# Kernel tuning notes

Measured on AMD Instinct MI355X. Metric: run time of the kernel, lower is better.

## Reference

```python
import jax, jax.numpy as jnp
import numpy as np

NUM_HEADS = 8
HEAD_DIM = 64
D_MODEL = NUM_HEADS * HEAD_DIM  # 512
B, T = 4, 2048


def setup_inputs() -> dict:
    key = jax.random.key(0)
    k1, k2 = jax.random.split(key)
    x = jax.random.normal(k1, (B, T, D_MODEL), dtype=jnp.float32)
    mask = jnp.ones((B, 1, T, T), dtype=jnp.float32)
    W = jax.random.normal(k2, (D_MODEL, 3 * D_MODEL), dtype=jnp.float32) * (D_MODEL ** -0.5)
    b = jnp.zeros((3 * D_MODEL,), dtype=jnp.float32)
    return {"x": x, "mask": mask, "W": W, "b": b}


def reference(x, mask, W, b):
    batch = x.shape[0]
    # fused QKV projection: [B, T, 3D]
    qkv = jnp.einsum("btd,de->bte", x, W) + b
    # NOTE: faithful to torch reshape [B, T, H, Hd, 3] -> the size-3 axis is innermost
    qkv = qkv.reshape(batch, -1, NUM_HEADS, HEAD_DIM, 3)
    qkv = jnp.transpose(qkv, (4, 0, 2, 1, 3))  # [3, B, H, T, Hd]
    q, k, v = qkv[0], qkv[1], qkv[2]
    logits = jnp.einsum("bhqd,bhkd->bhqk", q, k) / (HEAD_DIM ** 0.5)
    logits = logits + (1.0 - mask) * -10000.0
    w = jax.nn.softmax(logits, axis=-1)
    out = jnp.einsum("bhqk,bhkd->bhqd", w, v)  # [B, H, T, Hd]
    out = jnp.transpose(out, (0, 2, 1, 3)).reshape(batch, -1, NUM_HEADS * HEAD_DIM)
    return out
```

## Files before the change

### kernel.cpp

```cpp
#include <hip/hip_runtime.h>
#include <hip/hip_bf16.h>
#include <stdint.h>

#define B_   4
#define T_   2048
#define H_   8
#define HD_  64
#define DM_  512
#define N3_  1536

typedef short bf_el;
typedef __attribute__((ext_vector_type(8))) bf_el bfrag;
typedef __attribute__((ext_vector_type(4))) float ffrag;

#define SCALE_L2E  0.18033688011112043f
#define MASK_L2E   14426.950408889634f

static __device__ __forceinline__ unsigned short f2bf(float f) {
    union { float f; unsigned int i; } v; v.f = f;
    unsigned int r = v.i + 0x7fff + ((v.i >> 16) & 1);
    return (unsigned short)(r >> 16);
}
static __device__ __forceinline__ unsigned short f2bf_fast(float f) {
    union { float f; unsigned int i; } v; v.f = f;
    return (unsigned short)((v.i + 0x8000u) >> 16);
}

__global__ __launch_bounds__(256) void k_prep(const float* __restrict__ W,
                                              const float* __restrict__ X,
                                              const float* __restrict__ mask,
                                              unsigned short* __restrict__ Wt,
                                              unsigned short* __restrict__ Xb,
                                              int* __restrict__ flags4) {
    __shared__ __align__(16) unsigned short Ls[64 * 72];
    const int bid = blockIdx.x;
    const int tid = threadIdx.x;

    if (bid < 512) {
        const int R0 = bid * 16;
        const int mb = R0 >> 11;
        const int q0 = R0 & 2047;
        const int e  = mb * 32 + (q0 >> 6);
        const int part = (R0 >> 4) & 3;
        const int wave = tid >> 6, lane = tid & 63;
        unsigned int acc = 0u;
        const float* base = mask + (size_t)R0 * T_ + tid * 8;
#pragma unroll
        for (int rr = 0; rr < 16; ++rr) {
            const uint4 u0 = *(const uint4*)(base + (size_t)rr * T_);
            const uint4 u1 = *(const uint4*)(base + (size_t)rr * T_ + 4);
            acc |= (u0.x ^ 0x3F800000u) | (u0.y ^ 0x3F800000u) |
                   (u0.z ^ 0x3F800000u) | (u0.w ^ 0x3F800000u) |
                   (u1.x ^ 0x3F800000u) | (u1.y ^ 0x3F800000u) |
                   (u1.z ^ 0x3F800000u) | (u1.w ^ 0x3F800000u);
        }
        unsigned long long bal = __ballot(acc != 0u);
        if (lane < 8) {
            const int kt = wave * 8 + lane;
            flags4[(e * 32 + kt) * 4 + part] = ((bal >> (8 * lane)) & 0xFFULL) ? 1 : 0;
        }
        return;
    }
    if (bid < 768) {
        const int b2 = bid - 512;
        const float* src = X + (size_t)b2 * 16384;
        unsigned short* dst = Xb + (size_t)b2 * 16384;
#pragma unroll
        for (int j = 0; j < 8; ++j) {
            int idx = j * 512 + tid * 2;
            float4 f0 = *(const float4*)(src + idx * 4);
            float4 f1 = *(const float4*)(src + idx * 4 + 4);
            __align__(16) unsigned short t8[8];
            t8[0] = f2bf_fast(f0.x); t8[1] = f2bf_fast(f0.y);
            t8[2] = f2bf_fast(f0.z); t8[3] = f2bf_fast(f0.w);
            t8[4] = f2bf_fast(f1.x); t8[5] = f2bf_fast(f1.y);
            t8[6] = f2bf_fast(f1.z); t8[7] = f2bf_fast(f1.w);
            *(uint4*)(dst + idx * 4) = *(const uint4*)t8;
        }
        return;
    }
    {
        const int t  = bid - 768;
        const int n0 = (t % 24) * 64;
        const int k0 = (t / 24) * 64;
#pragma unroll
        for (int i = 0; i < 4; ++i) {
            int chunk = tid + i * 256;
            int k = chunk >> 4;
            int c = chunk & 15;
            float4 f = *(const float4*)(W + (size_t)(k0 + k) * N3_ + n0 + c * 4);
            unsigned short* p = Ls + k * 72 + c * 4;
            p[0] = f2bf(f.x); p[1] = f2bf(f.y); p[2] = f2bf(f.z); p[3] = f2bf(f.w);
        }
        __syncthreads();
        const int n = tid >> 2;
        const int g = tid & 3;
        __align__(16) unsigned short tmp[16];
#pragma unroll
        for (int i = 0; i < 16; ++i) tmp[i] = Ls[(g * 16 + i) * 72 + n];
        uint4* dst = (uint4*)(Wt + (size_t)(n0 + n) * DM_ + k0 + g * 16);
        dst[0] = *(const uint4*)(tmp);
        dst[1] = *(const uint4*)(tmp + 8);
    }
}

__global__ __launch_bounds__(256, 4) void k_gemm_qkv(const unsigned short* __restrict__ Xb,
                                                     const unsigned short* __restrict__ Wt,
                                                     const float* __restrict__ bias,
                                                     unsigned short* __restrict__ Qb,
                                                     unsigned short* __restrict__ Kb,
                                                     unsigned short* __restrict__ Vtb) {
    __shared__ __align__(16) unsigned short SH[12800];
    unsigned short* As = SH;
    unsigned short* Bs = SH + 2560;
    unsigned short* Cs = SH;

    const int tid  = threadIdx.x;
    const int wave = tid >> 6;
    const int lane = tid & 63;
    const int quad = lane >> 4;
    const int l16  = lane & 15;
    const int wm = wave >> 1, wn = wave & 1;
    const int h  = blockIdx.x >> 7;
    const int m0 = (blockIdx.x & 127) * 64;
    const int n0 = h * 192;

    float bvv[6];
#pragma unroll
    for (int ni = 0; ni < 6; ++ni) bvv[ni] = bias[n0 + wn * 96 + ni * 16 + l16];

    ffrag acc[2][6];
#pragma unroll
    for (int i = 0; i < 2; ++i)
#pragma unroll
        for (int j = 0; j < 6; ++j) acc[i][j] = (ffrag){0.f, 0.f, 0.f, 0.f};

    const int ar = tid >> 2, ac = tid & 3;
    const int br0 = tid >> 2, br1 = (tid + 256) >> 2, br2 = (tid + 512) >> 2;
    const int bc  = tid & 3;
    uint4 pa, pb0, pb1, pb2;

    pa  = *(const uint4*)(Xb + (size_t)(m0 + ar) * DM_ + ac * 8);
    pb0 = *(const uint4*)(Wt + (size_t)(n0 + br0) * DM_ + bc * 8);
    pb1 = *(const uint4*)(Wt + (size_t)(n0 + br1) * DM_ + bc * 8);
    pb2 = *(const uint4*)(Wt + (size_t)(n0 + br2) * DM_ + bc * 8);

    for (int kt = 0; kt < 16; ++kt) {
        __syncthreads();
        *(uint4*)(As + ar * 40 + ac * 8)  = pa;
        *(uint4*)(Bs + br0 * 40 + bc * 8) = pb0;
        *(uint4*)(Bs + br1 * 40 + bc * 8) = pb1;
        *(uint4*)(Bs + br2 * 40 + bc * 8) = pb2;
        __syncthreads();
        if (kt < 15) {
            const int ko = (kt + 1) * 32;
            pa  = *(const uint4*)(Xb + (size_t)(m0 + ar) * DM_ + ko + ac * 8);
            pb0 = *(const uint4*)(Wt + (size_t)(n0 + br0) * DM_ + ko + bc * 8);
            pb1 = *(const uint4*)(Wt + (size_t)(n0 + br1) * DM_ + ko + bc * 8);
            pb2 = *(const uint4*)(Wt + (size_t)(n0 + br2) * DM_ + ko + bc * 8);
        }
        bfrag af[2], bfr[6];
#pragma unroll
        for (int mi = 0; mi < 2; ++mi)
            af[mi] = *(const bfrag*)(As + (wm * 32 + mi * 16 + l16) * 40 + quad * 8);
#pragma unroll
        for (int ni = 0; ni < 6; ++ni)
            bfr[ni] = *(const bfrag*)(Bs + (wn * 96 + ni * 16 + l16) * 40 + quad * 8);
#pragma unroll
        for (int mi = 0; mi < 2; ++mi)
#pragma unroll
            for (int ni = 0; ni < 6; ++ni)
                acc[mi][ni] = __builtin_amdgcn_mfma_f32_16x16x32_bf16(af[mi], bfr[ni], acc[mi][ni], 0, 0, 0);
    }

    const int b  = m0 >> 11;
    const int tb = m0 & 2047;
    const size_t bh = (size_t)(b * 8 + h);
    float cscale[6];
#pragma unroll
    for (int ni = 0; ni < 6; ++ni) {
        int c = wn * 96 + ni * 16 + l16;
        cscale[ni] = (c % 3 == 0) ? SCALE_L2E : 1.0f;
    }
    __syncthreads();
#pragma unroll
    for (int mi = 0; mi < 2; ++mi)
#pragma unroll
        for (int ni = 0; ni < 6; ++ni)
#pragma unroll
            for (int reg = 0; reg < 4; ++reg) {
                int r = wm * 32 + mi * 16 + quad * 4 + reg;
                int c = wn * 96 + ni * 16 + l16;
                Cs[r * 200 + c] = f2bf_fast((acc[mi][ni][reg] + bvv[ni]) * cscale[ni]);
            }
    __syncthreads();
#pragma unroll
    for (int i = 0; i < 2; ++i) {
        int idx = tid + i * 256;
        int tl = idx >> 3, hc = (idx & 7) * 8;
        __align__(16) unsigned short tq[8], tk[8];
#pragma unroll
        for (int j = 0; j < 8; ++j) {
            tq[j] = Cs[tl * 200 + (hc + j) * 3 + 0];
            tk[j] = Cs[tl * 200 + (hc + j) * 3 + 1];
        }
        *(uint4*)(Qb + (bh * T_ + tb + tl) * HD_ + hc) = *(const uint4*)tq;
        *(uint4*)(Kb + (bh * T_ + tb + tl) * HD_ + hc) = *(const uint4*)tk;
    }
#pragma unroll
    for (int i = 0; i < 2; ++i) {
        int idx = tid + i * 256;
        int hd = idx >> 3, t8 = (idx & 7) * 8;
        __align__(16) unsigned short tv[8];
#pragma unroll
        for (int j = 0; j < 8; ++j)
            tv[j] = Cs[(t8 + j) * 200 + hd * 3 + 2];
        *(uint4*)(Vtb + (bh * HD_ + hd) * T_ + tb + t8) = *(const uint4*)tv;
    }
}

__global__ __launch_bounds__(256) void k_attn(const unsigned short* __restrict__ Q,
                                              const unsigned short* __restrict__ K,
                                              const unsigned short* __restrict__ Vt,
                                              const float* __restrict__ mask,
                                              const int4* __restrict__ flags4,
                                              float* __restrict__ out) {
    __shared__ __align__(16) unsigned short Ks[2][64 * 72];
    __shared__ __align__(16) unsigned short Vs[2][64 * 72];
    __shared__ __align__(16) unsigned short Ps[4][16 * 72];

    const int tid = threadIdx.x;
    const int wave = tid >> 6, lane = tid & 63;
    const int quad = lane >> 4, l16 = lane & 15;
    const int bh = blockIdx.x & 31, b = bh >> 3, h = bh & 7;
    const int qt = blockIdx.x >> 5;
    const int q0 = qt * 128;

    bfrag qf[2][2];
#pragma unroll
    for (int g = 0; g < 2; ++g) {
        size_t qrow = ((size_t)bh * T_ + q0 + wave * 32 + g * 16 + l16) * HD_;
        qf[g][0] = *(const bfrag*)(Q + qrow + quad * 8);
        qf[g][1] = *(const bfrag*)(Q + qrow + 32 + quad * 8);
    }
    float lsum[2][4] = {{0.f,0.f,0.f,0.f},{0.f,0.f,0.f,0.f}};
    ffrag of[2][4];
#pragma unroll
    for (int g = 0; g < 2; ++g)
#pragma unroll
        for (int nb = 0; nb < 4; ++nb) of[g][nb] = (ffrag){0.f, 0.f, 0.f, 0.f};

    const int e0 = b * 32 + qt * 2;
    const int e1 = e0 + 1;

    const int sr0 = tid >> 3, sr1 = (tid + 256) >> 3, sc = tid & 7;
    const unsigned short* Kbase = K  + (size_t)bh * T_ * HD_;
    const unsigned short* Vbase = Vt + (size_t)bh * HD_ * T_;

    uint4 kreg[2], vreg[2];
    kreg[0] = *(const uint4*)(Kbase + (size_t)sr0 * HD_ + sc * 8);
    kreg[1] = *(const uint4*)(Kbase + (size_t)sr1 * HD_ + sc * 8);
    vreg[0] = *(const uint4*)(Vbase + (size_t)sr0 * T_ + sc * 8);
    vreg[1] = *(const uint4*)(Vbase + (size_t)sr1 * T_ + sc * 8);
    *(uint4*)(&Ks[0][sr0 * 72 + sc * 8]) = kreg[0];
    *(uint4*)(&Ks[0][sr1 * 72 + sc * 8]) = kreg[1];
    *(uint4*)(&Vs[0][sr0 * 72 + sc * 8]) = vreg[0];
    *(uint4*)(&Vs[0][sr1 * 72 + sc * 8]) = vreg[1];
    __syncthreads();

    for (int kt = 0; kt < 32; ++kt) {
        const int cur = kt & 1;
        if (kt < 31) {
            const int kn = (kt + 1) * 64;
            kreg[0] = *(const uint4*)(Kbase + (size_t)(kn + sr0) * HD_ + sc * 8);
            kreg[1] = *(const uint4*)(Kbase + (size_t)(kn + sr1) * HD_ + sc * 8);
            vreg[0] = *(const uint4*)(Vbase + (size_t)sr0 * T_ + kn + sc * 8);
            vreg[1] = *(const uint4*)(Vbase + (size_t)sr1 * T_ + kn + sc * 8);
        }
        int4 F0 = flags4[e0 * 32 + kt];
        int4 F1 = flags4[e1 * 32 + kt];
        int fl[2];
        fl[0] = F0.x | F0.y | F0.z | F0.w;
        fl[1] = F1.x | F1.y | F1.z | F1.w;

        bfrag vf[2][4];
#pragma unroll
        for (int ks = 0; ks < 2; ++ks)
#pragma unroll
            for (int nb = 0; nb < 4; ++nb)
                vf[ks][nb] = *(const bfrag*)(&Vs[cur][(nb * 16 + l16) * 72 + (ks * 4 + quad) * 8]);

#pragma unroll
        for (int g = 0; g < 2; ++g) {
            ffrag sf[4];
#pragma unroll
            for (int ns = 0; ns < 4; ++ns) {
                ffrag a = (ffrag){0.f, 0.f, 0.f, 0.f};
#pragma unroll
                for (int ks = 0; ks < 2; ++ks) {
                    bfrag kf = *(const bfrag*)(&Ks[cur][(ns * 16 + l16) * 72 + (ks * 4 + quad) * 8]);
                    a = __builtin_amdgcn_mfma_f32_16x16x32_bf16(qf[g][ks], kf, a, 0, 0, 0);
                }
                sf[ns] = a;
            }
            if (fl[g]) {
#pragma unroll
                for (int reg = 0; reg < 4; ++reg) {
                    int tq = q0 + wave * 32 + g * 16 + quad * 4 + reg;
                    const float* mrow = mask + ((size_t)b * T_ + tq) * T_ + kt * 64;
#pragma unroll
                    for (int ns = 0; ns < 4; ++ns) {
                        float msk = mrow[ns * 16 + l16];
                        float p = __builtin_amdgcn_exp2f(
                            fmaf(msk, MASK_L2E, sf[ns][reg] - MASK_L2E));
                        lsum[g][reg] += p;
                        Ps[wave][(quad * 4 + reg) * 72 + ns * 16 + l16] = f2bf_fast(p);
                    }
                }
            } else {
#pragma unroll
                for (int reg = 0; reg < 4; ++reg) {
#pragma unroll
                    for (int ns = 0; ns < 4; ++ns) {
                        float p = __builtin_amdgcn_exp2f(sf[ns][reg]);
                        lsum[g][reg] += p;
                        Ps[wave][(quad * 4 + reg) * 72 + ns * 16 + l16] = f2bf_fast(p);
                    }
                }
            }
#pragma unroll
            for (int ks = 0; ks < 2; ++ks) {
                bfrag pf = *(const bfrag*)(&Ps[wave][l16 * 72 + (ks * 4 + quad) * 8]);
#pragma unroll
                for (int nb = 0; nb < 4; ++nb)
                    of[g][nb] = __builtin_amdgcn_mfma_f32_16x16x32_bf16(pf, vf[ks][nb], of[g][nb], 0, 0, 0);
            }
        }
        if (kt < 31) {
            const int nxt = cur ^ 1;
            *(uint4*)(&Ks[nxt][sr0 * 72 + sc * 8]) = kreg[0];
            *(uint4*)(&Ks[nxt][sr1 * 72 + sc * 8]) = kreg[1];
            *(uint4*)(&Vs[nxt][sr0 * 72 + sc * 8]) = vreg[0];
            *(uint4*)(&Vs[nxt][sr1 * 72 + sc * 8]) = vreg[1];
            __syncthreads();
        }
    }
#pragma unroll
    for (int g = 0; g < 2; ++g)
#pragma unroll
    for (int reg = 0; reg < 4; ++reg) {
        float s = lsum[g][reg];
#pragma unroll
        for (int d = 1; d < 16; d <<= 1) s += __shfl_xor(s, d, 64);
        float inv = 1.0f / s;
        int t = q0 + wave * 32 + g * 16 + quad * 4 + reg;
#pragma unroll
        for (int nb = 0; nb < 4; ++nb)
            out[((size_t)b * T_ + t) * DM_ + h * 64 + nb * 16 + l16] = of[g][nb][reg] * inv;
    }
}

extern "C" void kernel_launch(void* const* d_in, const int* in_sizes, int n_in,
                              void* d_out, int out_size, void* d_ws, size_t ws_size,
                              hipStream_t stream) {
    const float* X    = (const float*)d_in[0];
    const float* mask = (const float*)d_in[1];
    const float* W    = (const float*)d_in[2];
    const float* bias = (const float*)d_in[3];
    float* outp = (float*)d_out;

    char* ws = (char*)d_ws;
    unsigned short* Wt  = (unsigned short*)(ws);
    unsigned short* Xb  = (unsigned short*)(ws + 1572864);
    unsigned short* Qb  = (unsigned short*)(ws + 9961472);
    unsigned short* Kb  = (unsigned short*)(ws + 18350080);
    unsigned short* Vtb = (unsigned short*)(ws + 26738688);
    int*            flg = (int*)(ws + 35127296);

    k_prep     <<<dim3(960),  256, 0, stream>>>(W, X, mask, Wt, Xb, flg);
    k_gemm_qkv <<<dim3(1024), 256, 0, stream>>>(Xb, Wt, bias, Qb, Kb, Vtb);
    k_attn     <<<dim3(512),  256, 0, stream>>>(Qb, Kb, Vtb, mask, (const int4*)flg, outp);
}
```

Baseline: 216.9 us.

## Halve attention query tile, drop K/V double buffering, use atomic mask flags

The attention kernel now gives each block 64 query rows instead of 128, one 16-row group per wave. This doubles the grid to 1024 blocks and cuts register and LDS use, aiming for more parallelism and occupancy. The K/V register-prefetch double buffer is replaced by a single LDS buffer loaded synchronously, with two barriers per key tile. The per-part mask flags become one int per tile, set by atomicOr after a memset. In exchange, K/V are read from global memory twice as often, load latency is no longer overlapped with compute, and an extra memset launch is added.

```diff
diff --git a/kernel.cpp b/kernel.cpp
--- a/kernel.cpp
+++ b/kernel.cpp
@@ -31,7 +31,7 @@
                                               const float* __restrict__ mask,
                                               unsigned short* __restrict__ Wt,
                                               unsigned short* __restrict__ Xb,
-                                              int* __restrict__ flags4) {
+                                              int* __restrict__ flags) {
     __shared__ __align__(16) unsigned short Ls[64 * 72];
     const int bid = blockIdx.x;
     const int tid = threadIdx.x;
@@ -41,7 +41,6 @@
         const int mb = R0 >> 11;
         const int q0 = R0 & 2047;
         const int e  = mb * 32 + (q0 >> 6);
-        const int part = (R0 >> 4) & 3;
         const int wave = tid >> 6, lane = tid & 63;
         unsigned int acc = 0u;
         const float* base = mask + (size_t)R0 * T_ + tid * 8;
@@ -55,9 +54,11 @@
                    (u1.z ^ 0x3F800000u) | (u1.w ^ 0x3F800000u);
         }
         unsigned long long bal = __ballot(acc != 0u);
-        if (lane < 8) {
-            const int kt = wave * 8 + lane;
-            flags4[(e * 32 + kt) * 4 + part] = ((bal >> (8 * lane)) & 0xFFULL) ? 1 : 0;
+        if (lane == 0 && bal != 0ULL) {
+#pragma unroll
+            for (int j = 0; j < 8; ++j)
+                if ((bal >> (8 * j)) & 0xFFULL)
+                    atomicOr(&flags[e * 32 + wave * 8 + j], 1);
         }
         return;
     }
@@ -223,10 +224,10 @@
                                               const unsigned short* __restrict__ K,
                                               const unsigned short* __restrict__ Vt,
                                               const float* __restrict__ mask,
-                                              const int4* __restrict__ flags4,
+                                              const int* __restrict__ flags,
                                               float* __restrict__ out) {
-    __shared__ __align__(16) unsigned short Ks[2][64 * 72];
-    __shared__ __align__(16) unsigned short Vs[2][64 * 72];
+    __shared__ __align__(16) unsigned short Ks[64 * 72];
+    __shared__ __align__(16) unsigned short Vs[64 * 72];
     __shared__ __align__(16) unsigned short Ps[4][16 * 72];
 
     const int tid = threadIdx.x;
@@ -234,129 +235,95 @@
     const int quad = lane >> 4, l16 = lane & 15;
     const int bh = blockIdx.x & 31, b = bh >> 3, h = bh & 7;
     const int qt = blockIdx.x >> 5;
-    const int q0 = qt * 128;
-
-    bfrag qf[2][2];
-#pragma unroll
-    for (int g = 0; g < 2; ++g) {
-        size_t qrow = ((size_t)bh * T_ + q0 + wave * 32 + g * 16 + l16) * HD_;
-        qf[g][0] = *(const bfrag*)(Q + qrow + quad * 8);
-        qf[g][1] = *(const bfrag*)(Q + qrow + 32 + quad * 8);
-    }
-    float lsum[2][4] = {{0.f,0.f,0.f,0.f},{0.f,0.f,0.f,0.f}};
-    ffrag of[2][4];
-#pragma unroll
-    for (int g = 0; g < 2; ++g)
-#pragma unroll
-        for (int nb = 0; nb < 4; ++nb) of[g][nb] = (ffrag){0.f, 0.f, 0.f, 0.f};
-
-    const int e0 = b * 32 + qt * 2;
-    const int e1 = e0 + 1;
+    const int q0 = qt * 64;
+    const int fbase = (b * 32 + qt) * 32;
+
+    bfrag qf[2];
+    {
+        size_t qrow = ((size_t)bh * T_ + q0 + wave * 16 + l16) * HD_;
+        qf[0] = *(const bfrag*)(Q + qrow + quad * 8);
+        qf[1] = *(const bfrag*)(Q + qrow + 32 + quad * 8);
+    }
+    float lsum[4] = {0.f, 0.f, 0.f, 0.f};
+    ffrag of[4];
+#pragma unroll
+    for (int nb = 0; nb < 4; ++nb) of[nb] = (ffrag){0.f, 0.f, 0.f, 0.f};
 
     const int sr0 = tid >> 3, sr1 = (tid + 256) >> 3, sc = tid & 7;
     const unsigned short* Kbase = K  + (size_t)bh * T_ * HD_;
     const unsigned short* Vbase = Vt + (size_t)bh * HD_ * T_;
 
-    uint4 kreg[2], vreg[2];
-    kreg[0] = *(const uint4*)(Kbase + (size_t)sr0 * HD_ + sc * 8);
-    kreg[1] = *(const uint4*)(Kbase + (size_t)sr1 * HD_ + sc * 8);
-    vreg[0] = *(const uint4*)(Vbase + (size_t)sr0 * T_ + sc * 8);
-    vreg[1] = *(const uint4*)(Vbase + (size_t)sr1 * T_ + sc * 8);
-    *(uint4*)(&Ks[0][sr0 * 72 + sc * 8]) = kreg[0];
-    *(uint4*)(&Ks[0][sr1 * 72 + sc * 8]) = kreg[1];
-    *(uint4*)(&Vs[0][sr0 * 72 + sc * 8]) = vreg[0];
-    *(uint4*)(&Vs[0][sr1 * 72 + sc * 8]) = vreg[1];
-    __syncthreads();
-
     for (int kt = 0; kt < 32; ++kt) {
-        const int cur = kt & 1;
-        if (kt < 31) {
-            const int kn = (kt + 1) * 64;
-            kreg[0] = *(const uint4*)(Kbase + (size_t)(kn + sr0) * HD_ + sc * 8);
-            kreg[1] = *(const uint4*)(Kbase + (size_t)(kn + sr1) * HD_ + sc * 8);
-            vreg[0] = *(const uint4*)(Vbase + (size_t)sr0 * T_ + kn + sc * 8);
-            vreg[1] = *(const uint4*)(Vbase + (size_t)sr1 * T_ + kn + sc * 8);
-        }
-        int4 F0 = flags4[e0 * 32 + kt];
-        int4 F1 = flags4[e1 * 32 + kt];
-        int fl[2];
-        fl[0] = F0.x | F0.y | F0.z | F0.w;
-        fl[1] = F1.x | F1.y | F1.z | F1.w;
-
-        bfrag vf[2][4];
-#pragma unroll
-        for (int ks = 0; ks < 2; ++ks)
-#pragma unroll
-            for (int nb = 0; nb < 4; ++nb)
-                vf[ks][nb] = *(const bfrag*)(&Vs[cur][(nb * 16 + l16) * 72 + (ks * 4 + quad) * 8]);
-
-#pragma unroll
-        for (int g = 0; g < 2; ++g) {
-            ffrag sf[4];
-#pragma unroll
-            for (int ns = 0; ns < 4; ++ns) {
-                ffrag a = (ffrag){0.f, 0.f, 0.f, 0.f};
-#pragma unroll
-                for (int ks = 0; ks < 2; ++ks) {
-                    bfrag kf = *(const bfrag*)(&Ks[cur][(ns * 16 + l16) * 72 + (ks * 4 + quad) * 8]);
-                    a = __builtin_amdgcn_mfma_f32_16x16x32_bf16(qf[g][ks], kf, a, 0, 0, 0);
+        __syncthreads();
+        {
+            const int kn = kt * 64;
+            *(uint4*)(Ks + sr0 * 72 + sc * 8) =
+                *(const uint4*)(Kbase + (size_t)(kn + sr0) * HD_ + sc * 8);
+            *(uint4*)(Ks + sr1 * 72 + sc * 8) =
+                *(const uint4*)(Kbase + (size_t)(kn + sr1) * HD_ + sc * 8);
+            *(uint4*)(Vs + sr0 * 72 + sc * 8) =
+                *(const uint4*)(Vbase + (size_t)sr0 * T_ + kn + sc * 8);
+            *(uint4*)(Vs + sr1 * 72 + sc * 8) =
+                *(const uint4*)(Vbase + (size_t)sr1 * T_ + kn + sc * 8);
+        }
+        const int fl = flags[fbase + kt];
+        __syncthreads();
+        ffrag sf[4];
+#pragma unroll
+        for (int ns = 0; ns < 4; ++ns) {
+            ffrag a = (ffrag){0.f, 0.f, 0.f, 0.f};
+#pragma unroll
+            for (int ks = 0; ks < 2; ++ks) {
+                bfrag kf = *(const bfrag*)(Ks + (ns * 16 + l16) * 72 + (ks * 4 + quad) * 8);
+                a = __builtin_amdgcn_mfma_f32_16x16x32_bf16(qf[ks], kf, a, 0, 0, 0);
+            }
+            sf[ns] = a;
+        }
+        if (fl) {
+#pragma unroll
+            for (int reg = 0; reg < 4; ++reg) {
+                int tq = q0 + wave * 16 + quad * 4 + reg;
+                const float* mrow = mask + ((size_t)b * T_ + tq) * T_ + kt * 64;
+#pragma unroll
+                for (int ns = 0; ns < 4; ++ns) {
+                    float msk = mrow[ns * 16 + l16];
+                    float p = __builtin_amdgcn_exp2f(
+                        fmaf(msk, MASK_L2E, sf[ns][reg] - MASK_L2E));
+                    lsum[reg] += p;
+                    Ps[wave][(quad * 4 + reg) * 72 + ns * 16 + l16] = f2bf_fast(p);
                 }
-                sf[ns] = a;
-            }
-            if (fl[g]) {
-#pragma unroll
-                for (int reg = 0; reg < 4; ++reg) {
-                    int tq = q0 + wave * 32 + g * 16 + quad * 4 + reg;
-                    const float* mrow = mask + ((size_t)b * T_ + tq) * T_ + kt * 64;
-#pragma unroll
-                    for (int ns = 0; ns < 4; ++ns) {
-                        float msk = mrow[ns * 16 + l16];
-                        float p = __builtin_amdgcn_exp2f(
-                            fmaf(msk, MASK_L2E, sf[ns][reg] - MASK_L2E));
-                        lsum[g][reg] += p;
-                        Ps[wave][(quad * 4 + reg) * 72 + ns * 16 + l16] = f2bf_fast(p);
-                    }
+            }
+        } else {
+#pragma unroll
+            for (int reg = 0; reg < 4; ++reg) {
+#pragma unroll
+                for (int ns = 0; ns < 4; ++ns) {
+                    float p = __builtin_amdgcn_exp2f(sf[ns][reg]);
+                    lsum[reg] += p;
+                    Ps[wave][(quad * 4 + reg) * 72 + ns * 16 + l16] = f2bf_fast(p);
                 }
-            } else {
-#pragma unroll
-                for (int reg = 0; reg < 4; ++reg) {
-#pragma unroll
-                    for (int ns = 0; ns < 4; ++ns) {
-                        float p = __builtin_amdgcn_exp2f(sf[ns][reg]);
-                        lsum[g][reg] += p;
-                        Ps[wave][(quad * 4 + reg) * 72 + ns * 16 + l16] = f2bf_fast(p);
-                    }
-                }
-            }
-#pragma unroll
-            for (int ks = 0; ks < 2; ++ks) {
-                bfrag pf = *(const bfrag*)(&Ps[wave][l16 * 72 + (ks * 4 + quad) * 8]);
-#pragma unroll
-                for (int nb = 0; nb < 4; ++nb)
-                    of[g][nb] = __builtin_amdgcn_mfma_f32_16x16x32_bf16(pf, vf[ks][nb], of[g][nb], 0, 0, 0);
-            }
-        }
-        if (kt < 31) {
-            const int nxt = cur ^ 1;
-            *(uint4*)(&Ks[nxt][sr0 * 72 + sc * 8]) = kreg[0];
-            *(uint4*)(&Ks[nxt][sr1 * 72 + sc * 8]) = kreg[1];
-            *(uint4*)(&Vs[nxt][sr0 * 72 + sc * 8]) = vreg[0];
-            *(uint4*)(&Vs[nxt][sr1 * 72 + sc * 8]) = vreg[1];
-            __syncthreads();
-        }
-    }
-#pragma unroll
-    for (int g = 0; g < 2; ++g)
+            }
+        }
+#pragma unroll
+        for (int ks = 0; ks < 2; ++ks) {
+            bfrag pf = *(const bfrag*)(&Ps[wave][l16 * 72 + (ks * 4 + quad) * 8]);
+#pragma unroll
+            for (int nb = 0; nb < 4; ++nb) {
+                bfrag vf = *(const bfrag*)(Vs + (nb * 16 + l16) * 72 + (ks * 4 + quad) * 8);
+                of[nb] = __builtin_amdgcn_mfma_f32_16x16x32_bf16(pf, vf, of[nb], 0, 0, 0);
+            }
+        }
+    }
 #pragma unroll
     for (int reg = 0; reg < 4; ++reg) {
-        float s = lsum[g][reg];
+        float s = lsum[reg];
 #pragma unroll
         for (int d = 1; d < 16; d <<= 1) s += __shfl_xor(s, d, 64);
         float inv = 1.0f / s;
-        int t = q0 + wave * 32 + g * 16 + quad * 4 + reg;
+        int t = q0 + wave * 16 + quad * 4 + reg;
 #pragma unroll
         for (int nb = 0; nb < 4; ++nb)
-            out[((size_t)b * T_ + t) * DM_ + h * 64 + nb * 16 + l16] = of[g][nb][reg] * inv;
+            out[((size_t)b * T_ + t) * DM_ + h * 64 + nb * 16 + l16] = of[nb][reg] * inv;
     }
 }
 
@@ -377,7 +344,8 @@
     unsigned short* Vtb = (unsigned short*)(ws + 26738688);
     int*            flg = (int*)(ws + 35127296);
 
+    hipMemsetAsync(flg, 0, 16384, stream);
     k_prep     <<<dim3(960),  256, 0, stream>>>(W, X, mask, Wt, Xb, flg);
     k_gemm_qkv <<<dim3(1024), 256, 0, stream>>>(Xb, Wt, bias, Qb, Kb, Vtb);
-    k_attn     <<<dim3(512),  256, 0, stream>>>(Qb, Kb, Vtb, mask, (const int4*)flg, outp);
-}
+    k_attn     <<<dim3(1024), 256, 0, stream>>>(Qb, Kb, Vtb, mask, flg, outp);
+}
```

After: 224.0 us. 3.3% more time.
